# Kernel tuning notes

Measured on AMD Instinct MI355X. Metric: run time of the kernel, lower is better.

The kernel has to match this reference:

```python
import jax, jax.numpy as jnp
import numpy as np
import math

B = 2        # batch
S = 4095     # input sequence (cls token makes L = 4096)
F_IN = 32    # input feature size
D = 512      # d_model (hidden_size)
H = 8        # n_heads
E = D // H   # head dim = 64
DFF = 2048   # feedforward dim
NL = 2       # encoder layers
FACTOR = 5   # probsparse sampling factor
EPS = 1e-5


def setup_inputs() -> dict:
    key = jax.random.key(0)
    ks = jax.random.split(key, 16)

    def w(k, shape):
        return jax.random.normal(k, shape, dtype=jnp.float32) * 0.02

    inp = {}
    inp['x'] = jax.random.normal(ks[0], (B, S, F_IN), dtype=jnp.float32)
    inp['We'] = w(ks[1], (D, F_IN)); inp['be'] = jnp.zeros((D,), jnp.float32)
    inp['cls'] = jnp.zeros((1, 1, D), jnp.float32)
    inp['Wq'] = w(ks[2], (NL, D, D)); inp['bq'] = jnp.zeros((NL, D), jnp.float32)
    inp['Wk'] = w(ks[3], (NL, D, D)); inp['bk'] = jnp.zeros((NL, D), jnp.float32)
    inp['Wv'] = w(ks[4], (NL, D, D)); inp['bv'] = jnp.zeros((NL, D), jnp.float32)
    inp['Wo'] = w(ks[5], (NL, D, D)); inp['bo'] = jnp.zeros((NL, D), jnp.float32)
    inp['g1'] = jnp.ones((NL, D), jnp.float32); inp['b1'] = jnp.zeros((NL, D), jnp.float32)
    inp['g2'] = jnp.ones((NL, D), jnp.float32); inp['b2'] = jnp.zeros((NL, D), jnp.float32)
    inp['W1'] = w(ks[6], (NL, DFF, D)); inp['bf1'] = jnp.zeros((NL, DFF), jnp.float32)
    inp['W2'] = w(ks[7], (NL, D, DFF)); inp['bf2'] = jnp.zeros((NL, D), jnp.float32)
    inp['Wf'] = w(ks[8], (1, D)); inp['bf'] = jnp.zeros((1,), jnp.float32)
    return inp


def pos_encoding(L):
    # Sinusoidal positional encoding [L, D]
    pos = jnp.arange(L, dtype=jnp.float32)[:, None]
    div = jnp.exp(jnp.arange(0, D, 2, dtype=jnp.float32) * (-math.log(10000.0) / D))
    pe = jnp.zeros((L, D), jnp.float32)
    pe = pe.at[:, 0::2].set(jnp.sin(pos * div))
    pe = pe.at[:, 1::2].set(jnp.cos(pos * div))
    return pe


def layer_norm(x, g, b):
    mu = x.mean(-1, keepdims=True)
    var = ((x - mu) ** 2).mean(-1, keepdims=True)
    return (x - mu) / jnp.sqrt(var + EPS) * g + b


def prob_attention(q, k, v, rng):
    # q, k, v: [B, H, L, E]; mask_flag=False (encoder self-attention)
    b, h, L, e = q.shape
    u = min(FACTOR * int(np.ceil(np.log(L))), L)  # sample_k == n_top here (L_Q == L_K)
    idx = jax.random.randint(rng, (L, u), 0, L)   # random K sampling per query position
    Ks = k[:, :, idx, :]                          # [B,H,L,u,E] gather
    QKs = jnp.einsum('bhle,bhlue->bhlu', q, Ks)   # sampled scores
    M = QKs.max(-1) - QKs.sum(-1) / L             # sparsity measure [B,H,L]
    _, top = jax.lax.top_k(M, u)                  # active query indices [B,H,u]
    Qr = jnp.take_along_axis(q, top[..., None], axis=2)      # [B,H,u,E]
    scores = jnp.einsum('bhue,bhke->bhuk', Qr, k) / math.sqrt(e)
    attn = jax.nn.softmax(scores, axis=-1)
    ctx = jnp.broadcast_to(v.mean(axis=2, keepdims=True), (b, h, L, e))  # initial context = mean(V)
    upd = jnp.einsum('bhuk,bhke->bhue', attn, v)
    bi = jnp.arange(b)[:, None, None]
    hi = jnp.arange(h)[None, :, None]
    ctx = ctx.at[bi, hi, top].set(upd)            # scatter active-query contexts
    return ctx                                    # [B,H,L,E]


def attention_layer(x, Wq_, bq_, Wk_, bk_, Wv_, bv_, Wo_, bo_, rng):
    b, L, _ = x.shape
    q = (x @ Wq_.T + bq_).reshape(b, L, H, E).transpose(0, 2, 1, 3)
    k = (x @ Wk_.T + bk_).reshape(b, L, H, E).transpose(0, 2, 1, 3)
    v = (x @ Wv_.T + bv_).reshape(b, L, H, E).transpose(0, 2, 1, 3)
    ctx = prob_attention(q, k, v, rng)            # [B,H,L,E]
    out = ctx.transpose(0, 2, 1, 3).reshape(b, L, D)
    return out @ Wo_.T + bo_


def reference(x, We, be, cls, Wq, bq, Wk, bk, Wv, bv, Wo, bo, g1, b1, g2, b2, W1, bf1, W2, bf2, Wf, bf):
    h = x @ We.T + be                                            # [B,S,D]
    h = jnp.concatenate([jnp.broadcast_to(cls, (B, 1, D)), h], axis=1)  # prepend cls
    L = h.shape[1]
    h = h + pos_encoding(L)[None]
    for l in range(NL):
        rng = jax.random.fold_in(jax.random.key(42), l)
        a = attention_layer(h, Wq[l], bq[l], Wk[l], bk[l], Wv[l], bv[l], Wo[l], bo[l], rng)
        h = layer_norm(h + a, g1[l], b1[l])
        y = jax.nn.relu(h @ W1[l].T + bf1[l])
        y = y @ W2[l].T + bf2[l]
        h = layer_norm(h + y, g2[l], b2[l])
    return h[:, 0] @ Wf.T + bf  # cls-token prediction head [B,1]
```

## Files before the change

kernel.cpp:

```cpp
#include <hip/hip_runtime.h>
#include <hip/hip_bf16.h>
#include <math.h>
#include <stdint.h>

#define B 2
#define S 4095
#define LSEQ 4096
#define F_IN 32
#define D 512
#define H 8
#define E 64
#define DFF 2048
#define NL 2
#define U 45
#define EPSL 1e-5f
#define LU (LSEQ * U)
#define HALF_LU (LU / 2)
#define NS 32
#define SLICE 128

typedef __attribute__((ext_vector_type(8))) short short8;
typedef __attribute__((ext_vector_type(4))) float f32x4;

#define GLD(gp, lp)                                                            \
    __builtin_amdgcn_global_load_lds(                                          \
        (const __attribute__((address_space(1))) void*)(gp),                   \
        (__attribute__((address_space(3))) void*)(lp), 16, 0, 0)

__device__ __forceinline__ unsigned short bf16_bits(float f) {
    __hip_bfloat16 h = __float2bfloat16(f);
    return *(unsigned short*)&h;
}
__device__ __forceinline__ float bits_to_f32(unsigned short s) {
    union { uint32_t u; float f; } c;
    c.u = ((uint32_t)s) << 16;
    return c.f;
}
__device__ __forceinline__ unsigned long long mkey(float v, int index) {
    uint32_t u = __float_as_uint(v);
    uint32_t mono = (u & 0x80000000u) ? ~u : (u | 0x80000000u);
    return ((unsigned long long)mono << 32) | (uint32_t)(0xFFFFFFFFu - (uint32_t)index);
}

#define TF_BODY(k0, k1, c0, c1, o0, o1)                                        \
    do {                                                                       \
        uint32_t ks2 = (k0) ^ (k1) ^ 0x1BD11BDAu;                              \
        uint32_t x0 = (c0) + (k0), x1 = (c1) + (k1);                           \
        x0 += x1; x1 = ((x1 << 13) | (x1 >> 19)); x1 ^= x0;                    \
        x0 += x1; x1 = ((x1 << 15) | (x1 >> 17)); x1 ^= x0;                    \
        x0 += x1; x1 = ((x1 << 26) | (x1 >> 6));  x1 ^= x0;                    \
        x0 += x1; x1 = ((x1 << 6) | (x1 >> 26));  x1 ^= x0;                    \
        x0 += (k1); x1 += ks2 + 1u;                                            \
        x0 += x1; x1 = ((x1 << 17) | (x1 >> 15)); x1 ^= x0;                    \
        x0 += x1; x1 = ((x1 << 29) | (x1 >> 3));  x1 ^= x0;                    \
        x0 += x1; x1 = ((x1 << 16) | (x1 >> 16)); x1 ^= x0;                    \
        x0 += x1; x1 = ((x1 << 24) | (x1 >> 8));  x1 ^= x0;                    \
        x0 += ks2; x1 += (k0) + 2u;                                            \
        x0 += x1; x1 = ((x1 << 13) | (x1 >> 19)); x1 ^= x0;                    \
        x0 += x1; x1 = ((x1 << 15) | (x1 >> 17)); x1 ^= x0;                    \
        x0 += x1; x1 = ((x1 << 26) | (x1 >> 6));  x1 ^= x0;                    \
        x0 += x1; x1 = ((x1 << 6) | (x1 >> 26));  x1 ^= x0;                    \
        x0 += (k0); x1 += (k1) + 3u;                                           \
        x0 += x1; x1 = ((x1 << 17) | (x1 >> 15)); x1 ^= x0;                    \
        x0 += x1; x1 = ((x1 << 29) | (x1 >> 3));  x1 ^= x0;                    \
        x0 += x1; x1 = ((x1 << 16) | (x1 >> 16)); x1 ^= x0;                    \
        x0 += x1; x1 = ((x1 << 24) | (x1 >> 8));  x1 ^= x0;                    \
        x0 += (k1); x1 += ks2 + 4u;                                            \
        x0 += x1; x1 = ((x1 << 13) | (x1 >> 19)); x1 ^= x0;                    \
        x0 += x1; x1 = ((x1 << 15) | (x1 >> 17)); x1 ^= x0;                    \
        x0 += x1; x1 = ((x1 << 26) | (x1 >> 6));  x1 ^= x0;                    \
        x0 += x1; x1 = ((x1 << 6) | (x1 >> 26));  x1 ^= x0;                    \
        x0 += ks2; x1 += (k0) + 5u;                                            \
        (o0) = x0; (o1) = x1;                                                  \
    } while (0)

__device__ __forceinline__ void threefry_dev(uint32_t k0, uint32_t k1, uint32_t c0,
                                             uint32_t c1, uint32_t& o0, uint32_t& o1) {
    TF_BODY(k0, k1, c0, c1, o0, o1);
}
static void threefry_host(uint32_t k0, uint32_t k1, uint32_t c0, uint32_t c1,
                          uint32_t& o0, uint32_t& o1) {
    TF_BODY(k0, k1, c0, c1, o0, o1);
}

__global__ void prep_embed_kernel(const float* __restrict__ x, const float* __restrict__ We,
                                  __hip_bfloat16* __restrict__ xbf,
                                  __hip_bfloat16* __restrict__ webf) {
    int u = blockIdx.x * blockDim.x + threadIdx.x;
    const int NX = B * LSEQ * F_IN / 4;
    const int NW = D * F_IN / 4;
    if (u < NX) {
        int e0 = u * 4;
        int i = e0 & 31;
        int l = (e0 >> 5) & (LSEQ - 1);
        int b = e0 >> 17;
        union { unsigned short s[4]; uint2 w; } o;
        if (l == 0) {
            o.s[0] = o.s[1] = o.s[2] = o.s[3] = 0;
        } else {
            float4 v = *(const float4*)(x + ((size_t)b * S + (l - 1)) * F_IN + i);
            o.s[0] = bf16_bits(v.x); o.s[1] = bf16_bits(v.y);
            o.s[2] = bf16_bits(v.z); o.s[3] = bf16_bits(v.w);
        }
        ((uint2*)xbf)[u] = o.w;
    } else if (u < NX + NW) {
        int w = u - NX;
        float4 v = ((const float4*)We)[w];
        union { unsigned short s[4]; uint2 w2; } o;
        o.s[0] = bf16_bits(v.x); o.s[1] = bf16_bits(v.y);
        o.s[2] = bf16_bits(v.z); o.s[3] = bf16_bits(v.w);
        ((uint2*)webf)[w] = o.w2;
    }
}

__global__ __launch_bounds__(256) void gemm32(const unsigned short* __restrict__ A,
                                              const unsigned short* __restrict__ W,
                                              const float* __restrict__ bias,
                                              const float* __restrict__ cls,
                                              __hip_bfloat16* __restrict__ hbf,
                                              int M, int N, int K) {
    __shared__ unsigned short lds[2 * 128 * 32];
    unsigned short* As = lds;
    unsigned short* Bs = lds + 128 * 32;
    const int tid = threadIdx.x;
    const int m0 = blockIdx.y * 128, n0 = blockIdx.x * 128;
    const int wave = tid >> 6, lane = tid & 63;
    const int wm = (wave >> 1) * 64, wn = (wave & 1) * 64;
    const int quad = lane >> 4, m15 = lane & 15;
    const int srow = tid >> 2, scol = (tid & 3) * 8;
    f32x4 acc[4][4] = {};
    const unsigned short* Ag0 = A + (size_t)(m0 + srow) * K + scol;
    const unsigned short* Ag1 = A + (size_t)(m0 + srow + 64) * K + scol;
    const unsigned short* Wg0 = W + (size_t)(n0 + srow) * K + scol;
    const unsigned short* Wg1 = W + (size_t)(n0 + srow + 64) * K + scol;
    for (int k0 = 0; k0 < K; k0 += 32) {
        __syncthreads();
        GLD(Ag0 + k0, As + tid * 8);
        GLD(Ag1 + k0, As + 2048 + tid * 8);
        GLD(Wg0 + k0, Bs + tid * 8);
        GLD(Wg1 + k0, Bs + 2048 + tid * 8);
        __syncthreads();
        short8 af[4], bfr[4];
#pragma unroll
        for (int mi = 0; mi < 4; ++mi)
            af[mi] = *(const short8*)(As + (wm + mi * 16 + m15) * 32 + quad * 8);
#pragma unroll
        for (int ni = 0; ni < 4; ++ni)
            bfr[ni] = *(const short8*)(Bs + (wn + ni * 16 + m15) * 32 + quad * 8);
#pragma unroll
        for (int mi = 0; mi < 4; ++mi)
#pragma unroll
            for (int ni = 0; ni < 4; ++ni)
                acc[mi][ni] = __builtin_amdgcn_mfma_f32_16x16x32_bf16(
                    af[mi], bfr[ni], acc[mi][ni], 0, 0, 0);
    }
#pragma unroll
    for (int mi = 0; mi < 4; ++mi) {
        int mg = m0 + wm + mi * 16 + quad * 4;
#pragma unroll
        for (int ni = 0; ni < 4; ++ni) {
            int ng = n0 + wn + ni * 16 + m15;
            float bv = bias[ng];
            float cv = cls[ng];
            int i2 = ng >> 1;
            float divv = expf((float)(2 * i2) * (float)(-9.210340371976184 / 512.0));
#pragma unroll
            for (int r = 0; r < 4; ++r) {
                int row = mg + r;
                int l = row & (LSEQ - 1);
                float v = (l == 0) ? cv : (acc[mi][ni][r] + bv);
                float ang = (float)l * divv;
                v += (ng & 1) ? cosf(ang) : sinf(ang);
                hbf[(size_t)row * N + ng] = __float2bfloat16(v);
            }
        }
    }
}

__global__ void cast_weights_kernel(const float* __restrict__ Wq_l,
                                    const float* __restrict__ Wk_l,
                                    const float* __restrict__ Wv_l,
                                    const float* __restrict__ Wo_l,
                                    const float* __restrict__ W1_l,
                                    const float* __restrict__ W2_l,
                                    const float* __restrict__ bq_l,
                                    const float* __restrict__ bk_l,
                                    const float* __restrict__ bv_l,
                                    __hip_bfloat16* __restrict__ wqb,
                                    __hip_bfloat16* __restrict__ wkb,
                                    __hip_bfloat16* __restrict__ wvb,
                                    __hip_bfloat16* __restrict__ wob,
                                    __hip_bfloat16* __restrict__ w1b,
                                    __hip_bfloat16* __restrict__ w2b,
                                    float* __restrict__ qkvbias,
                                    unsigned char* __restrict__ flags) {
    const int SDD = D * D / 4;
    const int SFD = DFF * D / 4;
    const int CAST_N = 4 * SDD + 2 * SFD;
    int u = blockIdx.x * blockDim.x + threadIdx.x;
    if (u >= CAST_N) {
        int j = u - CAST_N;
        if (j < 384) {
            int seg = (j * 4) >> 9;
            int off = (j * 4) & 511;
            const float* src = (seg == 0) ? bq_l : (seg == 1) ? bk_l : bv_l;
            *(float4*)(qkvbias + j * 4) = *(const float4*)(src + off);
        } else if (j < 384 + B * LSEQ / 4) {
            ((int*)flags)[j - 384] = 0;
        }
        return;
    }
    const float* src;
    __hip_bfloat16* dst;
    int off;
    if (u < SDD) { src = Wq_l; dst = wqb; off = u; }
    else if (u < 2 * SDD) { src = Wk_l; dst = wkb; off = u - SDD; }
    else if (u < 3 * SDD) { src = Wv_l; dst = wvb; off = u - 2 * SDD; }
    else if (u < 4 * SDD) { src = Wo_l; dst = wob; off = u - 3 * SDD; }
    else if (u < 4 * SDD + SFD) { src = W1_l; dst = w1b; off = u - 4 * SDD; }
    else { src = W2_l; dst = w2b; off = u - 4 * SDD - SFD; }
    float4 v = ((const float4*)src)[off];
    union { unsigned short s[4]; uint2 w; } o;
    o.s[0] = bf16_bits(v.x); o.s[1] = bf16_bits(v.y);
    o.s[2] = bf16_bits(v.z); o.s[3] = bf16_bits(v.w);
    ((uint2*)dst)[off] = o.w;
}

template <int MODE>
__global__ __launch_bounds__(256) void gemm_pipe(const unsigned short* __restrict__ A,
                                                 const unsigned short* __restrict__ W,
                                                 const float* __restrict__ bias,
                                                 void* __restrict__ C0,
                                                 void* __restrict__ C1,
                                                 void* __restrict__ C2,
                                                 int M, int N, int K, int NBN) {
    __shared__ unsigned short As[2][128 * 32];
    __shared__ unsigned short Bs[2][128 * 32];
    const int tid = threadIdx.x;
    const int NBM = M >> 7;
    const int bid = blockIdx.x;
    const int xcd = bid & 7, local = bid >> 3;
    const int m_t = xcd * (NBM >> 3) + local / NBN;
    const int n_t = local % NBN;
    const int m0 = m_t * 128, n0 = n_t * 128;
    const int wave = tid >> 6, lane = tid & 63;
    const int wm = (wave >> 1) * 64, wn = (wave & 1) * 64;
    const int quad = lane >> 4, m15 = lane & 15;
    const int srow = tid >> 2, scol = (tid & 3) * 8;
    f32x4 acc[4][4] = {};
    const unsigned short* Ag0 = A + (size_t)(m0 + srow) * K + scol;
    const unsigned short* Ag1 = A + (size_t)(m0 + srow + 64) * K + scol;
    const unsigned short* Wg0 = W + (size_t)(n0 + srow) * K + scol;
    const unsigned short* Wg1 = W + (size_t)(n0 + srow + 64) * K + scol;
    GLD(Ag0, As[0] + tid * 8);
    GLD(Ag1, As[0] + 2048 + tid * 8);
    GLD(Wg0, Bs[0] + tid * 8);
    GLD(Wg1, Bs[0] + 2048 + tid * 8);
    int cur = 0;
    for (int k0 = 0; k0 < K; k0 += 32) {
        __syncthreads();
        int kn = k0 + 32;
        if (kn < K) {
            GLD(Ag0 + kn, As[cur ^ 1] + tid * 8);
            GLD(Ag1 + kn, As[cur ^ 1] + 2048 + tid * 8);
            GLD(Wg0 + kn, Bs[cur ^ 1] + tid * 8);
            GLD(Wg1 + kn, Bs[cur ^ 1] + 2048 + tid * 8);
        }
        short8 af[4], bfr[4];
#pragma unroll
        for (int mi = 0; mi < 4; ++mi)
            af[mi] = *(const short8*)(As[cur] + (wm + mi * 16 + m15) * 32 + quad * 8);
#pragma unroll
        for (int ni = 0; ni < 4; ++ni)
            bfr[ni] = *(const short8*)(Bs[cur] + (wn + ni * 16 + m15) * 32 + quad * 8);
#pragma unroll
        for (int mi = 0; mi < 4; ++mi)
#pragma unroll
            for (int ni = 0; ni < 4; ++ni)
                acc[mi][ni] = __builtin_amdgcn_mfma_f32_16x16x32_bf16(
                    af[mi], bfr[ni], acc[mi][ni], 0, 0, 0);
        cur ^= 1;
    }
#pragma unroll
    for (int mi = 0; mi < 4; ++mi) {
        int mg = m0 + wm + mi * 16 + quad * 4;
#pragma unroll
        for (int ni = 0; ni < 4; ++ni) {
            int ng = n0 + wn + ni * 16 + m15;
            float bv = bias[ng];
#pragma unroll
            for (int r = 0; r < 4; ++r) {
                float v = acc[mi][ni][r] + bv;
                if (MODE == 1) {
                    ((__hip_bfloat16*)C0)[(size_t)(mg + r) * N + ng] = __float2bfloat16(v);
                } else if (MODE == 2) {
                    ((__hip_bfloat16*)C0)[(size_t)(mg + r) * N + ng] =
                        __float2bfloat16(fmaxf(v, 0.f));
                } else {
                    int seg = ng >> 9;
                    int col = ng & 511;
                    __hip_bfloat16* dst = (seg == 0) ? (__hip_bfloat16*)C0
                                        : (seg == 1) ? (__hip_bfloat16*)C1
                                                     : (__hip_bfloat16*)C2;
                    dst[(size_t)(mg + r) * D + col] = __float2bfloat16(v);
                }
            }
        }
    }
}

__global__ __launch_bounds__(256) void gemm_w2b(const unsigned short* __restrict__ A,
                                                const unsigned short* __restrict__ W,
                                                const float* __restrict__ bias,
                                                float* __restrict__ C0,
                                                float* __restrict__ C1) {
    const int K = 2048, N = 512, KH = 1024;
    __shared__ unsigned short As[2][128 * 32];
    __shared__ unsigned short Bs[2][128 * 32];
    const int tid = threadIdx.x;
    const int bid = blockIdx.x;
    const int xcd = bid & 7, local = bid >> 3;
    const int m_t = xcd * 8 + (local >> 3);
    const int n_t = (local >> 1) & 3;
    const int ks = local & 1;
    const int m0 = m_t * 128, n0 = n_t * 128, kb = ks * KH;
    const int wave = tid >> 6, lane = tid & 63;
    const int wm = (wave >> 1) * 64, wn = (wave & 1) * 64;
    const int quad = lane >> 4, m15 = lane & 15;
    const int srow = tid >> 2, scol = (tid & 3) * 8;
    f32x4 acc[4][4] = {};
    const unsigned short* Ag0 = A + (size_t)(m0 + srow) * K + kb + scol;
    const unsigned short* Ag1 = A + (size_t)(m0 + srow + 64) * K + kb + scol;
    const unsigned short* Wg0 = W + (size_t)(n0 + srow) * K + kb + scol;
    const unsigned short* Wg1 = W + (size_t)(n0 + srow + 64) * K + kb + scol;
    GLD(Ag0, As[0] + tid * 8);
    GLD(Ag1, As[0] + 2048 + tid * 8);
    GLD(Wg0, Bs[0] + tid * 8);
    GLD(Wg1, Bs[0] + 2048 + tid * 8);
    int cur = 0;
    for (int k0 = 0; k0 < KH; k0 += 32) {
        __syncthreads();
        int kn = k0 + 32;
        if (kn < KH) {
            GLD(Ag0 + kn, As[cur ^ 1] + tid * 8);
            GLD(Ag1 + kn, As[cur ^ 1] + 2048 + tid * 8);
            GLD(Wg0 + kn, Bs[cur ^ 1] + tid * 8);
            GLD(Wg1 + kn, Bs[cur ^ 1] + 2048 + tid * 8);
        }
        short8 af[4], bfr[4];
#pragma unroll
        for (int mi = 0; mi < 4; ++mi)
            af[mi] = *(const short8*)(As[cur] + (wm + mi * 16 + m15) * 32 + quad * 8);
#pragma unroll
        for (int ni = 0; ni < 4; ++ni)
            bfr[ni] = *(const short8*)(Bs[cur] + (wn + ni * 16 + m15) * 32 + quad * 8);
#pragma unroll
        for (int mi = 0; mi < 4; ++mi)
#pragma unroll
            for (int ni = 0; ni < 4; ++ni)
                acc[mi][ni] = __builtin_amdgcn_mfma_f32_16x16x32_bf16(
                    af[mi], bfr[ni], acc[mi][ni], 0, 0, 0);
        cur ^= 1;
    }
    float* Cf = ks ? C1 : C0;
#pragma unroll
    for (int mi = 0; mi < 4; ++mi) {
        int mg = m0 + wm + mi * 16 + quad * 4;
#pragma unroll
        for (int ni = 0; ni < 4; ++ni) {
            int ng = n0 + wn + ni * 16 + m15;
            float bv = ks ? 0.f : bias[ng];
#pragma unroll
            for (int r = 0; r < 4; ++r)
                Cf[(size_t)(mg + r) * N + ng] = acc[mi][ni][r] + bv;
        }
    }
}

__global__ __launch_bounds__(256) void mscore_kernel(const __hip_bfloat16* __restrict__ qbf,
                                                     const __hip_bfloat16* __restrict__ kbf,
                                                     uint32_t k2a, uint32_t k2b,
                                                     float* __restrict__ Mv) {
    __shared__ float Sbuf[U][8];
    __shared__ int sidx[U];
    int bid = blockIdx.x;
    int b = bid & 1;
    int l = bid >> 1;
    int tid = threadIdx.x;
    int wave = tid >> 6, lane = tid & 63;
    if (tid < U) {
        int i = l * U + tid;
        uint32_t c0 = (i < HALF_LU) ? (uint32_t)i : (uint32_t)(i - HALF_LU);
        uint32_t o0, o1;
        threefry_dev(k2a, k2b, c0, c0 + HALF_LU, o0, o1);
        sidx[tid] = (int)(((i < HALF_LU) ? o0 : o1) & 4095u);
    }
    const unsigned short* qr =
        (const unsigned short*)qbf + ((size_t)(b * LSEQ) + l) * D + lane * 8;
    union { uint4 u; unsigned short s[8]; } qv;
    qv.u = *(const uint4*)qr;
    float qa[8];
#pragma unroll
    for (int j = 0; j < 8; ++j) qa[j] = bits_to_f32(qv.s[j]);
    __syncthreads();
    const unsigned short* kbase = (const unsigned short*)(kbf + (size_t)(b * LSEQ) * D);
    for (int t = wave; t < U; t += 4) {
        int kr = sidx[t];
        union { uint4 u; unsigned short s[8]; } kv;
        kv.u = *(const uint4*)(kbase + (size_t)kr * D + lane * 8);
        float p = 0.f;
#pragma unroll
        for (int j = 0; j < 8; ++j) p += qa[j] * bits_to_f32(kv.s[j]);
        p += __shfl_xor(p, 1);
        p += __shfl_xor(p, 2);
        p += __shfl_xor(p, 4);
        if ((lane & 7) == 0) Sbuf[t][lane >> 3] = p;
    }
    __syncthreads();
    if (tid < 8) {
        float mx = -INFINITY, sm = 0.f;
        for (int t = 0; t < U; ++t) {
            float v = Sbuf[t][tid];
            mx = fmaxf(mx, v);
            sm += v;
        }
        Mv[((size_t)b * H + tid) * LSEQ + l] = mx - sm / (float)LSEQ;
    }
}

__global__ __launch_bounds__(256) void topk_chunk_kernel(const float* __restrict__ Mv,
                                                         unsigned long long* __restrict__ cand) {
    __shared__ unsigned long long sk[256];
    int blk = blockIdx.x;
    int chunk = blk & 15, bh = blk >> 4;
    int tid = threadIdx.x;
    int gi = chunk * 256 + tid;
    sk[tid] = mkey(Mv[(size_t)bh * LSEQ + gi], gi);
    __syncthreads();
    for (int k = 2; k <= 256; k <<= 1) {
        for (int j = k >> 1; j > 0; j >>= 1) {
            int ixj = tid ^ j;
            if (ixj > tid) {
                unsigned long long a = sk[tid], b = sk[ixj];
                bool desc = ((tid & k) == 0);
                if (desc ? (a < b) : (a > b)) { sk[tid] = b; sk[ixj] = a; }
            }
            __syncthreads();
        }
    }
    if (tid < U) cand[((size_t)bh * 16 + chunk) * U + tid] = sk[tid];
}

__global__ __launch_bounds__(256) void topk_merge_kernel(const unsigned long long* __restrict__ cand,
                                                         int* __restrict__ top) {
    __shared__ unsigned long long sk[1024];
    int bh = blockIdx.x;
    int tid = threadIdx.x;
    for (int e = tid; e < 1024; e += 256)
        sk[e] = (e < 16 * U) ? cand[(size_t)bh * 16 * U + e] : 0ull;
    __syncthreads();
    for (int k = 2; k <= 1024; k <<= 1) {
        for (int j = k >> 1; j > 0; j >>= 1) {
            for (int e = tid; e < 1024; e += 256) {
                int ixj = e ^ j;
                if (ixj > e) {
                    unsigned long long a = sk[e], b = sk[ixj];
                    bool desc = ((e & k) == 0);
                    if (desc ? (a < b) : (a > b)) { sk[e] = b; sk[ixj] = a; }
                }
            }
            __syncthreads();
        }
    }
    if (tid < U)
        top[bh * U + tid] = (int)(0xFFFFFFFFu - (uint32_t)(sk[tid] & 0xFFFFFFFFu));
}

__global__ __launch_bounds__(256) void vmean_part(const __hip_bfloat16* __restrict__ v,
                                                  float* __restrict__ part) {
    int blk = blockIdx.x;
    int seg = blk & 7, hh = (blk >> 3) & 7, b = blk >> 6;
    int e = threadIdx.x & 63, rg = threadIdx.x >> 6;
    const __hip_bfloat16* vp =
        v + ((size_t)(b * LSEQ) + seg * 512) * D + hh * 64 + e;
    float acc = 0.f;
    for (int r = rg; r < 512; r += 4) acc += __bfloat162float(vp[(size_t)r * D]);
    __shared__ float red[4][64];
    red[rg][e] = acc;
    __syncthreads();
    if (threadIdx.x < 64)
        part[(size_t)blk * 64 + threadIdx.x] =
            red[0][threadIdx.x] + red[1][threadIdx.x] + red[2][threadIdx.x] + red[3][threadIdx.x];
}

__global__ void vmean_reduce(const float* __restrict__ part, float* __restrict__ vm) {
    int gid = blockIdx.x * blockDim.x + threadIdx.x;
    if (gid >= B * H * E) return;
    int e = gid & 63, bh = gid >> 6;
    float acc = 0.f;
#pragma unroll
    for (int s = 0; s < 8; ++s) acc += part[((size_t)bh * 8 + s) * 64 + e];
    vm[gid] = acc / (float)LSEQ;
}

__global__ __launch_bounds__(256) void wo_base_kernel(const float* __restrict__ vm,
                                                      const unsigned short* __restrict__ wob,
                                                      const float* __restrict__ bo,
                                                      float* __restrict__ base) {
    int b = blockIdx.x >> 7;
    int n = (blockIdx.x & 127) * 4 + (threadIdx.x >> 6);
    int lane = threadIdx.x & 63;
    const float* vmr = vm + (size_t)b * D + lane * 8;
    float4 va = *(const float4*)vmr;
    float4 vb = *(const float4*)(vmr + 4);
    union { uint4 u; unsigned short s[8]; } w;
    w.u = *(const uint4*)(wob + (size_t)n * D + lane * 8);
    float p = va.x * bits_to_f32(w.s[0]) + va.y * bits_to_f32(w.s[1]) +
              va.z * bits_to_f32(w.s[2]) + va.w * bits_to_f32(w.s[3]) +
              vb.x * bits_to_f32(w.s[4]) + vb.y * bits_to_f32(w.s[5]) +
              vb.z * bits_to_f32(w.s[6]) + vb.w * bits_to_f32(w.s[7]);
    for (int off = 32; off; off >>= 1) p += __shfl_xor(p, off);
    if (lane == 0) base[(size_t)b * D + n] = p + bo[n];
}

__global__ __launch_bounds__(128) void zero_corr_kernel(const int* __restrict__ top,
                                                        float* __restrict__ aout,
                                                        unsigned char* __restrict__ flags) {
    int bid = blockIdx.x;
    int t = bid % U;
    int bh = bid / U;
    int b = bh >> 3;
    int r = top[bh * U + t];
    int tid = threadIdx.x;
    float4 z = {0.f, 0.f, 0.f, 0.f};
    ((float4*)(aout + (size_t)(b * LSEQ + r) * D))[tid] = z;
    if (tid == 0) flags[b * LSEQ + r] = 1;
}

__global__ __launch_bounds__(256) void attnred_corr_kernel(const float* __restrict__ Opart,
                                                           const float* __restrict__ msum,
                                                           const float* __restrict__ vm,
                                                           const unsigned short* __restrict__ wob,
                                                           const int* __restrict__ top,
                                                           float* __restrict__ aout) {
    __shared__ float dlt[E];
    int bid = blockIdx.x;
    int t = bid % U;
    int bh = bid / U;
    int b = bh >> 3, hh = bh & 7;
    int tid = threadIdx.x;
    if (tid < 64) {
        int lane = tid;
        float m_s = -INFINITY, ss = 0.f;
        if (lane < NS) {
            size_t base = (((size_t)bh * NS + lane) * U + t) * 2;
            m_s = msum[base];
            ss = msum[base + 1];
        }
        float M = m_s;
        for (int off = 32; off; off >>= 1) M = fmaxf(M, __shfl_xor(M, off));
        float e_s = (lane < NS) ? __expf(m_s - M) : 0.f;
        float d = ss * e_s;
        for (int off = 32; off; off >>= 1) d += __shfl_xor(d, off);
        float acc = 0.f;
        for (int s = 0; s < NS; ++s) {
            float w = __shfl(e_s, s);
            acc += w * Opart[(((size_t)bh * NS + s) * U + t) * 64 + lane];
        }
        dlt[lane] = acc / d - vm[(size_t)bh * E + lane];
    }
    __syncthreads();
    int r = top[bh * U + t];
    float* arow = aout + (size_t)(b * LSEQ + r) * D;
    for (int n = tid; n < D; n += 256) {
        const unsigned short* wr = wob + (size_t)n * D + hh * E;
        float acc = 0.f;
#pragma unroll
        for (int k2 = 0; k2 < E; ++k2) acc += dlt[k2] * bits_to_f32(wr[k2]);
        atomicAdd(arow + n, acc);
    }
}

__global__ __launch_bounds__(256) void attn_part(const __hip_bfloat16* __restrict__ qbf,
                                                 const __hip_bfloat16* __restrict__ kbf,
                                                 const __hip_bfloat16* __restrict__ vbf,
                                                 const int* __restrict__ top,
                                                 float* __restrict__ Opart,
                                                 float* __restrict__ msum) {
    __shared__ unsigned short Qs[48 * 72];
    __shared__ unsigned short Ks[SLICE * 72];
    __shared__ unsigned short Vs[SLICE * 68];
    __shared__ unsigned short Ps[48 * 136];
    __shared__ float mred[48][4];
    __shared__ float sred[48][4];
    const int slice = blockIdx.x, hh = blockIdx.y, b = blockIdx.z;
    const int bh = b * H + hh;
    const int tid = threadIdx.x;
    const int s0 = slice * SLICE;
    for (int i = tid; i < 48 * 64; i += 256) {
        int t = i >> 6, e = i & 63;
        unsigned short v = 0;
        if (t < U) {
            int r = top[bh * U + t];
            v = ((const unsigned short*)qbf)[((size_t)(b * LSEQ) + r) * D + hh * E + e];
        }
        Qs[t * 72 + e] = v;
    }
    {
        const uint4* src = (const uint4*)(kbf + ((size_t)(b * LSEQ) + s0) * D + hh * E);
        for (int i = tid; i < SLICE * 8; i += 256) {
            int r = i >> 3, c = i & 7;
            uint4 d = src[(size_t)r * 64 + c];
            *(uint4*)(Ks + r * 72 + c * 8) = d;
        }
    }
    {
        const uint2* src = (const uint2*)(vbf + ((size_t)(b * LSEQ) + s0) * D + hh * E);
        for (int i = tid; i < SLICE * 16; i += 256) {
            int r = i >> 4, c = i & 15;
            uint2 d = src[(size_t)r * 128 + c];
            *(uint2*)(Vs + r * 68 + c * 4) = d;
        }
    }
    __syncthreads();
    const int wave = tid >> 6, lane = tid & 63;
    const int quad = lane >> 4, m15 = lane & 15;
    const int wc = wave * 32;
    f32x4 acc[3][2] = {};
#pragma unroll
    for (int ks = 0; ks < 2; ++ks) {
        short8 af[3], bfr[2];
#pragma unroll
        for (int mt = 0; mt < 3; ++mt)
            af[mt] = *(const short8*)(Qs + (mt * 16 + m15) * 72 + ks * 32 + quad * 8);
#pragma unroll
        for (int nt = 0; nt < 2; ++nt)
            bfr[nt] = *(const short8*)(Ks + (wc + nt * 16 + m15) * 72 + ks * 32 + quad * 8);
#pragma unroll
        for (int mt = 0; mt < 3; ++mt)
#pragma unroll
            for (int nt = 0; nt < 2; ++nt)
                acc[mt][nt] = __builtin_amdgcn_mfma_f32_16x16x32_bf16(
                    af[mt], bfr[nt], acc[mt][nt], 0, 0, 0);
    }
    float sc[3][2][4];
#pragma unroll
    for (int mt = 0; mt < 3; ++mt)
#pragma unroll
        for (int nt = 0; nt < 2; ++nt)
#pragma unroll
            for (int r = 0; r < 4; ++r) sc[mt][nt][r] = acc[mt][nt][r] * 0.125f;
#pragma unroll
    for (int mt = 0; mt < 3; ++mt)
#pragma unroll
        for (int r = 0; r < 4; ++r) {
            float mv = fmaxf(sc[mt][0][r], sc[mt][1][r]);
            mv = fmaxf(mv, __shfl_xor(mv, 1));
            mv = fmaxf(mv, __shfl_xor(mv, 2));
            mv = fmaxf(mv, __shfl_xor(mv, 4));
            mv = fmaxf(mv, __shfl_xor(mv, 8));
            if (m15 == 0) mred[mt * 16 + quad * 4 + r][wave] = mv;
        }
    __syncthreads();
#pragma unroll
    for (int mt = 0; mt < 3; ++mt)
#pragma unroll
        for (int r = 0; r < 4; ++r) {
            int row = mt * 16 + quad * 4 + r;
            float ms = fmaxf(fmaxf(mred[row][0], mred[row][1]),
                             fmaxf(mred[row][2], mred[row][3]));
            float p0 = __expf(sc[mt][0][r] - ms);
            float p1 = __expf(sc[mt][1][r] - ms);
            float sv = p0 + p1;
            sv += __shfl_xor(sv, 1);
            sv += __shfl_xor(sv, 2);
            sv += __shfl_xor(sv, 4);
            sv += __shfl_xor(sv, 8);
            if (m15 == 0) sred[row][wave] = sv;
            Ps[row * 136 + wc + m15] = bf16_bits(p0);
            Ps[row * 136 + wc + 16 + m15] = bf16_bits(p1);
        }
    __syncthreads();
    if (tid < U) {
        float mm = fmaxf(fmaxf(mred[tid][0], mred[tid][1]),
                         fmaxf(mred[tid][2], mred[tid][3]));
        float ss = sred[tid][0] + sred[tid][1] + sred[tid][2] + sred[tid][3];
        size_t base = (((size_t)bh * NS + slice) * U + tid) * 2;
        msum[base] = mm;
        msum[base + 1] = ss;
    }
    f32x4 apv[3] = {};
#pragma unroll
    for (int ks = 0; ks < 4; ++ks) {
        short8 bv;
#pragma unroll
        for (int j = 0; j < 8; ++j)
            bv[j] = (short)Vs[(ks * 32 + quad * 8 + j) * 68 + wave * 16 + m15];
        short8 af2[3];
#pragma unroll
        for (int mt = 0; mt < 3; ++mt)
            af2[mt] = *(const short8*)(Ps + (mt * 16 + m15) * 136 + ks * 32 + quad * 8);
#pragma unroll
        for (int mt = 0; mt < 3; ++mt)
            apv[mt] = __builtin_amdgcn_mfma_f32_16x16x32_bf16(af2[mt], bv, apv[mt], 0, 0, 0);
    }
    size_t obase = ((size_t)bh * NS + slice) * U;
#pragma unroll
    for (int mt = 0; mt < 3; ++mt)
#pragma unroll
        for (int r = 0; r < 4; ++r) {
            int row = mt * 16 + quad * 4 + r;
            if (row < U)
                Opart[(obase + row) * 64 + wave * 16 + m15] = apv[mt][r];
        }
}

__global__ __launch_bounds__(64) void add_ln_base_kernel(__hip_bfloat16* __restrict__ hbf,
                                                         const float* __restrict__ base,
                                                         const float* __restrict__ aout,
                                                         const unsigned char* __restrict__ flags,
                                                         const float* __restrict__ g,
                                                         const float* __restrict__ bb) {
    int row = blockIdx.x;
    int b = row >> 12;
    int lane = threadIdx.x;
    unsigned short* hp = (unsigned short*)hbf + (size_t)row * D;
    const float* bp = base + (size_t)b * D;
    const float* ap = aout + (size_t)row * D;
    bool has = flags[row] != 0;
    float x[8];
    float sum = 0.f;
#pragma unroll
    for (int j = 0; j < 8; ++j) {
        float a = bp[lane + 64 * j];
        if (has) a += ap[lane + 64 * j];
        x[j] = bits_to_f32(hp[lane + 64 * j]) + a;
        sum += x[j];
    }
    for (int off = 32; off; off >>= 1) sum += __shfl_xor(sum, off);
    float mu = sum / (float)D;
    float vs = 0.f;
#pragma unroll
    for (int j = 0; j < 8; ++j) {
        float dd = x[j] - mu;
        vs += dd * dd;
    }
    for (int off = 32; off; off >>= 1) vs += __shfl_xor(vs, off);
    float inv = 1.f / sqrtf(vs / (float)D + EPSL);
#pragma unroll
    for (int j = 0; j < 8; ++j) {
        float o = (x[j] - mu) * inv * g[lane + 64 * j] + bb[lane + 64 * j];
        hp[lane + 64 * j] = bf16_bits(o);
    }
}

__global__ __launch_bounds__(64) void add_ln_kernel(__hip_bfloat16* __restrict__ hbf,
                                                    const float* __restrict__ a,
                                                    const float* __restrict__ a2,
                                                    const float* __restrict__ g,
                                                    const float* __restrict__ bb) {
    int row = blockIdx.x;
    int lane = threadIdx.x;
    unsigned short* hp = (unsigned short*)hbf + (size_t)row * D;
    const float* ap = a + (size_t)row * D;
    const float* ap2 = a2 + (size_t)row * D;
    float x[8];
    float sum = 0.f;
#pragma unroll
    for (int j = 0; j < 8; ++j) {
        x[j] = bits_to_f32(hp[lane + 64 * j]) + ap[lane + 64 * j] + ap2[lane + 64 * j];
        sum += x[j];
    }
    for (int off = 32; off; off >>= 1) sum += __shfl_xor(sum, off);
    float mu = sum / (float)D;
    float vs = 0.f;
#pragma unroll
    for (int j = 0; j < 8; ++j) {
        float dd = x[j] - mu;
        vs += dd * dd;
    }
    for (int off = 32; off; off >>= 1) vs += __shfl_xor(vs, off);
    float inv = 1.f / sqrtf(vs / (float)D + EPSL);
#pragma unroll
    for (int j = 0; j < 8; ++j) {
        float o = (x[j] - mu) * inv * g[lane + 64 * j] + bb[lane + 64 * j];
        hp[lane + 64 * j] = bf16_bits(o);
    }
}

__global__ void final_kernel(const __hip_bfloat16* __restrict__ hbf,
                             const float* __restrict__ Wf,
                             const float* __restrict__ bf, float* __restrict__ out) {
    int b = blockIdx.x;
    int lane = threadIdx.x;
    const unsigned short* hp = (const unsigned short*)hbf + (size_t)b * LSEQ * D;
    float acc = 0.f;
    for (int j = lane; j < D; j += 64) acc += bits_to_f32(hp[j]) * Wf[j];
    for (int off = 32; off; off >>= 1) acc += __shfl_xor(acc, off);
    if (lane == 0) out[b] = acc + bf[0];
}

extern "C" void kernel_launch(void* const* d_in, const int* in_sizes, int n_in,
                              void* d_out, int out_size, void* d_ws, size_t ws_size,
                              hipStream_t stream) {
    (void)in_sizes; (void)n_in; (void)out_size; (void)ws_size;
    const float* x   = (const float*)d_in[0];
    const float* We  = (const float*)d_in[1];
    const float* be  = (const float*)d_in[2];
    const float* cls = (const float*)d_in[3];
    const float* Wq  = (const float*)d_in[4];
    const float* bq  = (const float*)d_in[5];
    const float* Wk  = (const float*)d_in[6];
    const float* bk  = (const float*)d_in[7];
    const float* Wv  = (const float*)d_in[8];
    const float* bv  = (const float*)d_in[9];
    const float* Wo  = (const float*)d_in[10];
    const float* bo  = (const float*)d_in[11];
    const float* g1  = (const float*)d_in[12];
    const float* b1  = (const float*)d_in[13];
    const float* g2  = (const float*)d_in[14];
    const float* b2  = (const float*)d_in[15];
    const float* W1  = (const float*)d_in[16];
    const float* bf1 = (const float*)d_in[17];
    const float* W2  = (const float*)d_in[18];
    const float* bf2 = (const float*)d_in[19];
    const float* Wf  = (const float*)d_in[20];
    const float* bff = (const float*)d_in[21];
    float* out = (float*)d_out;

    float* ws = (float*)d_ws;
    const size_t NT = (size_t)B * LSEQ * D;
    float* aout = ws + NT;
    __hip_bfloat16* kbf    = (__hip_bfloat16*)(ws + NT);
    __hip_bfloat16* q_bf   = (__hip_bfloat16*)(ws + 2 * NT);
    __hip_bfloat16* y1_bf  = (__hip_bfloat16*)(ws + 2 * NT);
    __hip_bfloat16* v_bf   = (__hip_bfloat16*)(ws + 4 * NT);
    __hip_bfloat16* h_bf   = (__hip_bfloat16*)(ws + 5 * NT);
    float* tmp  = ws;
    float* Opart = ws + 3 * NT;
    float* msumb = Opart + (size_t)B * H * NS * U * 64;
    float* wpool = ws + 5 * NT + NT / 2;
    __hip_bfloat16* wqb = (__hip_bfloat16*)wpool;
    __hip_bfloat16* wkb = wqb + (size_t)D * D;
    __hip_bfloat16* wvb = wkb + (size_t)D * D;
    __hip_bfloat16* wob = wvb + (size_t)D * D;
    __hip_bfloat16* w1b = wob + (size_t)D * D;
    __hip_bfloat16* w2b = w1b + (size_t)DFF * D;
    float* after_w = wpool + ((size_t)4 * D * D + 2 * (size_t)DFF * D) / 2;
    float* Mbuf = after_w;
    int* top    = (int*)(Mbuf + (size_t)B * H * LSEQ);
    float* vm   = (float*)(top + B * H * U);
    float* vpart  = vm + (size_t)B * H * E;
    float* baseb  = vpart + (size_t)128 * 64;
    __hip_bfloat16* xbf  = (__hip_bfloat16*)(baseb + (size_t)B * D);
    __hip_bfloat16* webf = xbf + (size_t)B * LSEQ * F_IN;
    unsigned long long* cand =
        (unsigned long long*)(((uintptr_t)(webf + (size_t)D * F_IN) + 7) & ~(uintptr_t)7);
    float* qkvbias = (float*)(cand + (size_t)B * H * 16 * U);
    unsigned char* flags = (unsigned char*)(qkvbias + 1536);

    const int ML = B * LSEQ;
    dim3 gD(D / 128, ML / 128);
    const int CAST_N = 4 * (D * D / 4) + 2 * (DFF * D / 4);
    const int CAST_TOT = CAST_N + 384 + B * LSEQ / 4;

    prep_embed_kernel<<<(B * LSEQ * F_IN / 4 + D * F_IN / 4 + 255) / 256, 256, 0, stream>>>(
        x, We, xbf, webf);
    gemm32<<<gD, 256, 0, stream>>>((const unsigned short*)xbf,
                                   (const unsigned short*)webf, be, cls, h_bf, ML, D, F_IN);

    for (int l = 0; l < NL; ++l) {
        uint32_t f0, f1, a0, a1, bb0, bb1;
        threefry_host(0u, 42u, 0u, (uint32_t)l, f0, f1);
        threefry_host(f0, f1, 0u, 2u, a0, a1);
        threefry_host(f0, f1, 1u, 3u, bb0, bb1);
        (void)a0; (void)bb0;

        cast_weights_kernel<<<(CAST_TOT + 255) / 256, 256, 0, stream>>>(
            Wq + (size_t)l * D * D, Wk + (size_t)l * D * D, Wv + (size_t)l * D * D,
            Wo + (size_t)l * D * D, W1 + (size_t)l * DFF * D, W2 + (size_t)l * D * DFF,
            bq + l * D, bk + l * D, bv + l * D,
            wqb, wkb, wvb, wob, w1b, w2b, qkvbias, flags);

        gemm_pipe<3><<<768, 256, 0, stream>>>((const unsigned short*)h_bf,
                                              (const unsigned short*)wqb, qkvbias,
                                              q_bf, kbf, v_bf, ML, 3 * D, D, 12);

        mscore_kernel<<<B * LSEQ, 256, 0, stream>>>(q_bf, kbf, a1, bb1, Mbuf);
        topk_chunk_kernel<<<B * H * 16, 256, 0, stream>>>(Mbuf, cand);
        topk_merge_kernel<<<B * H, 256, 0, stream>>>(cand, top);
        vmean_part<<<B * H * 8, 256, 0, stream>>>(v_bf, vpart);
        vmean_reduce<<<4, 256, 0, stream>>>(vpart, vm);
        wo_base_kernel<<<B * 128, 256, 0, stream>>>(vm, (const unsigned short*)wob,
                                                    bo + l * D, baseb);
        attn_part<<<dim3(NS, H, B), 256, 0, stream>>>(q_bf, kbf, v_bf, top, Opart, msumb);
        zero_corr_kernel<<<B * H * U, 128, 0, stream>>>(top, aout, flags);
        attnred_corr_kernel<<<B * H * U, 256, 0, stream>>>(Opart, msumb, vm,
                                                           (const unsigned short*)wob, top,
                                                           aout);
        add_ln_base_kernel<<<ML, 64, 0, stream>>>(h_bf, baseb, aout, flags,
                                                  g1 + l * D, b1 + l * D);

        gemm_pipe<2><<<1024, 256, 0, stream>>>((const unsigned short*)h_bf,
                                               (const unsigned short*)w1b, bf1 + l * DFF,
                                               y1_bf, nullptr, nullptr, ML, DFF, D, 16);
        gemm_w2b<<<512, 256, 0, stream>>>((const unsigned short*)y1_bf,
                                          (const unsigned short*)w2b, bf2 + l * D,
                                          aout, tmp);
        add_ln_kernel<<<ML, 64, 0, stream>>>(h_bf, aout, tmp, g2 + l * D, b2 + l * D);
    }

    final_kernel<<<B, 64, 0, stream>>>(h_bf, Wf, bff, out);
}
```

Measured before the change: 647.7 us.

## Merge small attention-side kernels and split positional encoding out of embed GEMM

Merges top-k merge with the V-mean partial sums into one launch, and merges zeroing of the correction rows with the Wo base projection. The separate vmean_reduce kernel goes away, because consumers now reduce the partial sums inline. Fewer per-layer launches and serialisation points is the intended gain. Separately, the embedding GEMM now writes fp32 to a workspace and a new elementwise kernel adds cls and the positional encoding. That adds one extra full-size fp32 round trip and one more launch at the start.

```diff
diff --git a/kernel.cpp b/kernel.cpp
--- a/kernel.cpp
+++ b/kernel.cpp
@@ -116,8 +116,7 @@
 __global__ __launch_bounds__(256) void gemm32(const unsigned short* __restrict__ A,
                                               const unsigned short* __restrict__ W,
                                               const float* __restrict__ bias,
-                                              const float* __restrict__ cls,
-                                              __hip_bfloat16* __restrict__ hbf,
+                                              float* __restrict__ Cf,
                                               int M, int N, int K) {
     __shared__ unsigned short lds[2 * 128 * 32];
     unsigned short* As = lds;
@@ -161,20 +160,25 @@
         for (int ni = 0; ni < 4; ++ni) {
             int ng = n0 + wn + ni * 16 + m15;
             float bv = bias[ng];
-            float cv = cls[ng];
-            int i2 = ng >> 1;
-            float divv = expf((float)(2 * i2) * (float)(-9.210340371976184 / 512.0));
-#pragma unroll
-            for (int r = 0; r < 4; ++r) {
-                int row = mg + r;
-                int l = row & (LSEQ - 1);
-                float v = (l == 0) ? cv : (acc[mi][ni][r] + bv);
-                float ang = (float)l * divv;
-                v += (ng & 1) ? cosf(ang) : sinf(ang);
-                hbf[(size_t)row * N + ng] = __float2bfloat16(v);
-            }
-        }
-    }
+#pragma unroll
+            for (int r = 0; r < 4; ++r)
+                Cf[(size_t)(mg + r) * N + ng] = acc[mi][ni][r] + bv;
+        }
+    }
+}
+
+__global__ void posenc_kernel(const float* __restrict__ emb, const float* __restrict__ cls,
+                              __hip_bfloat16* __restrict__ hbf) {
+    int gid = blockIdx.x * blockDim.x + threadIdx.x;
+    if (gid >= B * LSEQ * D) return;
+    int d = gid % D;
+    int l = (gid / D) % LSEQ;
+    float v = (l == 0) ? cls[d] : emb[gid];
+    int i = d >> 1;
+    float divv = expf((float)(2 * i) * (float)(-9.210340371976184 / 512.0));
+    float ang = (float)l * divv;
+    v += (d & 1) ? cosf(ang) : sinf(ang);
+    hbf[gid] = __float2bfloat16(v);
 }
 
 __global__ void cast_weights_kernel(const float* __restrict__ Wq_l,
@@ -451,95 +455,96 @@
     if (tid < U) cand[((size_t)bh * 16 + chunk) * U + tid] = sk[tid];
 }
 
-__global__ __launch_bounds__(256) void topk_merge_kernel(const unsigned long long* __restrict__ cand,
-                                                         int* __restrict__ top) {
+__global__ __launch_bounds__(256) void topkmerge_vmean_kernel(
+        const unsigned long long* __restrict__ cand, int* __restrict__ top,
+        const __hip_bfloat16* __restrict__ v, float* __restrict__ part) {
     __shared__ unsigned long long sk[1024];
-    int bh = blockIdx.x;
+    __shared__ float red[4][64];
+    int blk = blockIdx.x;
     int tid = threadIdx.x;
-    for (int e = tid; e < 1024; e += 256)
-        sk[e] = (e < 16 * U) ? cand[(size_t)bh * 16 * U + e] : 0ull;
-    __syncthreads();
-    for (int k = 2; k <= 1024; k <<= 1) {
-        for (int j = k >> 1; j > 0; j >>= 1) {
-            for (int e = tid; e < 1024; e += 256) {
-                int ixj = e ^ j;
-                if (ixj > e) {
-                    unsigned long long a = sk[e], b = sk[ixj];
-                    bool desc = ((e & k) == 0);
-                    if (desc ? (a < b) : (a > b)) { sk[e] = b; sk[ixj] = a; }
+    if (blk < B * H) {
+        int bh = blk;
+        for (int e = tid; e < 1024; e += 256)
+            sk[e] = (e < 16 * U) ? cand[(size_t)bh * 16 * U + e] : 0ull;
+        __syncthreads();
+        for (int k = 2; k <= 1024; k <<= 1) {
+            for (int j = k >> 1; j > 0; j >>= 1) {
+                for (int e = tid; e < 1024; e += 256) {
+                    int ixj = e ^ j;
+                    if (ixj > e) {
+                        unsigned long long a = sk[e], b = sk[ixj];
+                        bool desc = ((e & k) == 0);
+                        if (desc ? (a < b) : (a > b)) { sk[e] = b; sk[ixj] = a; }
+                    }
                 }
+                __syncthreads();
             }
-            __syncthreads();
-        }
-    }
-    if (tid < U)
-        top[bh * U + tid] = (int)(0xFFFFFFFFu - (uint32_t)(sk[tid] & 0xFFFFFFFFu));
-}
-
-__global__ __launch_bounds__(256) void vmean_part(const __hip_bfloat16* __restrict__ v,
-                                                  float* __restrict__ part) {
-    int blk = blockIdx.x;
-    int seg = blk & 7, hh = (blk >> 3) & 7, b = blk >> 6;
-    int e = threadIdx.x & 63, rg = threadIdx.x >> 6;
-    const __hip_bfloat16* vp =
-        v + ((size_t)(b * LSEQ) + seg * 512) * D + hh * 64 + e;
-    float acc = 0.f;
-    for (int r = rg; r < 512; r += 4) acc += __bfloat162float(vp[(size_t)r * D]);
-    __shared__ float red[4][64];
-    red[rg][e] = acc;
-    __syncthreads();
-    if (threadIdx.x < 64)
-        part[(size_t)blk * 64 + threadIdx.x] =
-            red[0][threadIdx.x] + red[1][threadIdx.x] + red[2][threadIdx.x] + red[3][threadIdx.x];
-}
-
-__global__ void vmean_reduce(const float* __restrict__ part, float* __restrict__ vm) {
-    int gid = blockIdx.x * blockDim.x + threadIdx.x;
-    if (gid >= B * H * E) return;
-    int e = gid & 63, bh = gid >> 6;
-    float acc = 0.f;
-#pragma unroll
-    for (int s = 0; s < 8; ++s) acc += part[((size_t)bh * 8 + s) * 64 + e];
-    vm[gid] = acc / (float)LSEQ;
-}
-
-__global__ __launch_bounds__(256) void wo_base_kernel(const float* __restrict__ vm,
-                                                      const unsigned short* __restrict__ wob,
-                                                      const float* __restrict__ bo,
-                                                      float* __restrict__ base) {
-    int b = blockIdx.x >> 7;
-    int n = (blockIdx.x & 127) * 4 + (threadIdx.x >> 6);
-    int lane = threadIdx.x & 63;
-    const float* vmr = vm + (size_t)b * D + lane * 8;
-    float4 va = *(const float4*)vmr;
-    float4 vb = *(const float4*)(vmr + 4);
-    union { uint4 u; unsigned short s[8]; } w;
-    w.u = *(const uint4*)(wob + (size_t)n * D + lane * 8);
-    float p = va.x * bits_to_f32(w.s[0]) + va.y * bits_to_f32(w.s[1]) +
-              va.z * bits_to_f32(w.s[2]) + va.w * bits_to_f32(w.s[3]) +
-              vb.x * bits_to_f32(w.s[4]) + vb.y * bits_to_f32(w.s[5]) +
-              vb.z * bits_to_f32(w.s[6]) + vb.w * bits_to_f32(w.s[7]);
-    for (int off = 32; off; off >>= 1) p += __shfl_xor(p, off);
-    if (lane == 0) base[(size_t)b * D + n] = p + bo[n];
-}
-
-__global__ __launch_bounds__(128) void zero_corr_kernel(const int* __restrict__ top,
-                                                        float* __restrict__ aout,
-                                                        unsigned char* __restrict__ flags) {
+        }
+        if (tid < U)
+            top[bh * U + tid] = (int)(0xFFFFFFFFu - (uint32_t)(sk[tid] & 0xFFFFFFFFu));
+    } else {
+        int vb = blk - B * H;
+        int seg = vb & 7, hh = (vb >> 3) & 7, b = vb >> 6;
+        int e = tid & 63, rg = tid >> 6;
+        const __hip_bfloat16* vp =
+            v + ((size_t)(b * LSEQ) + seg * 512) * D + hh * 64 + e;
+        float acc = 0.f;
+        for (int r = rg; r < 512; r += 4) acc += __bfloat162float(vp[(size_t)r * D]);
+        red[rg][e] = acc;
+        __syncthreads();
+        if (tid < 64)
+            part[(size_t)vb * 64 + tid] =
+                red[0][tid] + red[1][tid] + red[2][tid] + red[3][tid];
+    }
+}
+
+__global__ __launch_bounds__(256) void zero_wobase_kernel(
+        const int* __restrict__ top, float* __restrict__ aout,
+        unsigned char* __restrict__ flags, const float* __restrict__ vpart,
+        const unsigned short* __restrict__ wob, const float* __restrict__ bo,
+        float* __restrict__ base) {
     int bid = blockIdx.x;
-    int t = bid % U;
-    int bh = bid / U;
-    int b = bh >> 3;
-    int r = top[bh * U + t];
     int tid = threadIdx.x;
-    float4 z = {0.f, 0.f, 0.f, 0.f};
-    ((float4*)(aout + (size_t)(b * LSEQ + r) * D))[tid] = z;
-    if (tid == 0) flags[b * LSEQ + r] = 1;
+    if (bid < B * H * U) {
+        int t = bid % U;
+        int bh = bid / U;
+        int b = bh >> 3;
+        int r = top[bh * U + t];
+        if (tid < 128) {
+            float4 z = {0.f, 0.f, 0.f, 0.f};
+            ((float4*)(aout + (size_t)(b * LSEQ + r) * D))[tid] = z;
+        }
+        if (tid == 0) flags[b * LSEQ + r] = 1;
+    } else {
+        int wb = bid - B * H * U;
+        int b = wb >> 7;
+        int n = (wb & 127) * 4 + (tid >> 6);
+        int lane = tid & 63;
+        float vmv[8];
+#pragma unroll
+        for (int j = 0; j < 8; ++j) {
+            int idx = lane * 8 + j;
+            int hh = idx >> 6, e = idx & 63;
+            float acc = 0.f;
+#pragma unroll
+            for (int s = 0; s < 8; ++s)
+                acc += vpart[((size_t)(b * 8 + hh) * 8 + s) * 64 + e];
+            vmv[j] = acc / (float)LSEQ;
+        }
+        union { uint4 u; unsigned short s[8]; } w;
+        w.u = *(const uint4*)(wob + (size_t)n * D + lane * 8);
+        float p = vmv[0] * bits_to_f32(w.s[0]) + vmv[1] * bits_to_f32(w.s[1]) +
+                  vmv[2] * bits_to_f32(w.s[2]) + vmv[3] * bits_to_f32(w.s[3]) +
+                  vmv[4] * bits_to_f32(w.s[4]) + vmv[5] * bits_to_f32(w.s[5]) +
+                  vmv[6] * bits_to_f32(w.s[6]) + vmv[7] * bits_to_f32(w.s[7]);
+        for (int off = 32; off; off >>= 1) p += __shfl_xor(p, off);
+        if (lane == 0) base[(size_t)b * D + n] = p + bo[n];
+    }
 }
 
 __global__ __launch_bounds__(256) void attnred_corr_kernel(const float* __restrict__ Opart,
                                                            const float* __restrict__ msum,
-                                                           const float* __restrict__ vm,
+                                                           const float* __restrict__ vpart,
                                                            const unsigned short* __restrict__ wob,
                                                            const int* __restrict__ top,
                                                            float* __restrict__ aout) {
@@ -567,7 +572,10 @@
             float w = __shfl(e_s, s);
             acc += w * Opart[(((size_t)bh * NS + s) * U + t) * 64 + lane];
         }
-        dlt[lane] = acc / d - vm[(size_t)bh * E + lane];
+        float vmv = 0.f;
+#pragma unroll
+        for (int s = 0; s < 8; ++s) vmv += vpart[((size_t)bh * 8 + s) * 64 + lane];
+        dlt[lane] = acc / d - vmv / (float)LSEQ;
     }
     __syncthreads();
     int r = top[bh * U + t];
@@ -836,6 +844,7 @@
     __hip_bfloat16* y1_bf  = (__hip_bfloat16*)(ws + 2 * NT);
     __hip_bfloat16* v_bf   = (__hip_bfloat16*)(ws + 4 * NT);
     __hip_bfloat16* h_bf   = (__hip_bfloat16*)(ws + 5 * NT);
+    float* emb  = ws;
     float* tmp  = ws;
     float* Opart = ws + 3 * NT;
     float* msumb = Opart + (size_t)B * H * NS * U * 64;
@@ -867,7 +876,8 @@
     prep_embed_kernel<<<(B * LSEQ * F_IN / 4 + D * F_IN / 4 + 255) / 256, 256, 0, stream>>>(
         x, We, xbf, webf);
     gemm32<<<gD, 256, 0, stream>>>((const unsigned short*)xbf,
-                                   (const unsigned short*)webf, be, cls, h_bf, ML, D, F_IN);
+                                   (const unsigned short*)webf, be, emb, ML, D, F_IN);
+    posenc_kernel<<<(B * LSEQ * D + 255) / 256, 256, 0, stream>>>(emb, cls, h_bf);
 
     for (int l = 0; l < NL; ++l) {
         uint32_t f0, f1, a0, a1, bb0, bb1;
@@ -888,14 +898,12 @@
 
         mscore_kernel<<<B * LSEQ, 256, 0, stream>>>(q_bf, kbf, a1, bb1, Mbuf);
         topk_chunk_kernel<<<B * H * 16, 256, 0, stream>>>(Mbuf, cand);
-        topk_merge_kernel<<<B * H, 256, 0, stream>>>(cand, top);
-        vmean_part<<<B * H * 8, 256, 0, stream>>>(v_bf, vpart);
-        vmean_reduce<<<4, 256, 0, stream>>>(vpart, vm);
-        wo_base_kernel<<<B * 128, 256, 0, stream>>>(vm, (const unsigned short*)wob,
-                                                    bo + l * D, baseb);
+        topkmerge_vmean_kernel<<<B * H + B * H * 8, 256, 0, stream>>>(cand, top, v_bf,
+                                                                      vpart);
         attn_part<<<dim3(NS, H, B), 256, 0, stream>>>(q_bf, kbf, v_bf, top, Opart, msumb);
-        zero_corr_kernel<<<B * H * U, 128, 0, stream>>>(top, aout, flags);
-        attnred_corr_kernel<<<B * H * U, 256, 0, stream>>>(Opart, msumb, vm,
+        zero_wobase_kernel<<<B * H * U + B * 128, 256, 0, stream>>>(
+            top, aout, flags, vpart, (const unsigned short*)wob, bo + l * D, baseb);
+        attnred_corr_kernel<<<B * H * U, 256, 0, stream>>>(Opart, msumb, vpart,
                                                            (const unsigned short*)wob, top,
                                                            aout);
         add_ln_base_kernel<<<ML, 64, 0, stream>>>(h_bf, baseb, aout, flags,
```

Measured after the change: 553.0 us. 1.17x faster.
